# Optimization experiments

Hardware: AMD Instinct MI355X
Metric: run time of the kernel (lower is better)

The kernel has to match this reference:

```python
import jax, jax.numpy as jnp
import numpy as np


def _sliding_window_attention(q, k, v, window_size, padding_mask):
    # q,k,v: [B,H,S,D]; faithful to the torch code incl. clamped scatter_add
    # duplicates at boundaries and the (score==0 -> -inf) quirk.
    B, H, S, D = q.shape
    hw = window_size // 2
    kp = jnp.pad(k, ((0, 0), (0, 0), (hw, hw), (0, 0)))  # zero-pad seq dim
    # window gather positions into padded keys: [S, W+1]
    pos = jnp.arange(S)[:, None] + jnp.arange(window_size + 1)[None, :]
    kw = kp[:, :, pos, :]  # [B,H,S,W+1,D]
    scores = jnp.einsum('bhsd,bhswd->bhsw', q, kw) / jnp.sqrt(jnp.asarray(D, q.dtype))
    # scatter-add into full [B,H,S,S] with clamped column indices (duplicates sum)
    idx = jnp.clip(jnp.arange(S)[:, None] + jnp.arange(-hw, hw + 1)[None, :], 0, S - 1)  # [S,W+1]
    rows = jnp.arange(S)[:, None]
    full = jnp.zeros((B, H, S, S), q.dtype).at[:, :, rows, idx].add(scores)
    neg_inf = jnp.asarray(-jnp.inf, full.dtype)
    full = jnp.where(full == 0.0, neg_inf, full)
    if padding_mask is not None:
        pm = padding_mask[:, None, None, :]  # [B,1,1,S]
        full = jnp.where(pm == 0, neg_inf, full)
        full = jnp.where(jnp.swapaxes(pm, -1, -2) == 0, neg_inf, full)
    att = jax.nn.softmax(full, axis=-1)
    att = jnp.where(jnp.isnan(att), jnp.asarray(0.0, att.dtype), att)
    values = jnp.einsum('bhst,bhtd->bhsd', att, v)
    return values, att


def setup_inputs() -> dict:
    key = jax.random.key(0)
    ks = jax.random.split(key, 5)
    B, S, IN_DIM, E = 2, 2048, 512, 512
    x = jax.random.normal(ks[0], (B, S, IN_DIM), dtype=jnp.float32)
    padding_mask = jnp.ones((B, S), dtype=jnp.int32)
    qkv_w = jax.random.normal(ks[1], (3 * E, IN_DIM), dtype=jnp.float32) * 0.02
    qkv_b = jnp.zeros((3 * E,), dtype=jnp.float32)
    o_w = jax.random.normal(ks[2], (E, E), dtype=jnp.float32) * 0.02
    o_b = jnp.zeros((E,), dtype=jnp.float32)
    return {'x': x, 'padding_mask': padding_mask, 'qkv_w': qkv_w, 'qkv_b': qkv_b,
            'o_w': o_w, 'o_b': o_b, 'window_size': 256, 'num_heads': 8}


def reference(x, padding_mask, qkv_w, qkv_b, o_w, o_b, window_size, num_heads):
    B, S, _ = x.shape
    E3 = qkv_w.shape[0]
    E = E3 // 3
    head_dim = E // num_heads
    qkv = x @ qkv_w.T + qkv_b                         # [B,S,3E]
    qkv = qkv.reshape(B, S, num_heads, 3 * head_dim)
    qkv = jnp.transpose(qkv, (0, 2, 1, 3))            # [B,H,S,3*hd]
    q, k, v = jnp.split(qkv, 3, axis=-1)
    values, _ = _sliding_window_attention(q, k, v, window_size, padding_mask)
    values = jnp.transpose(values, (0, 2, 1, 3)).reshape(B, S, E)
    o = values @ o_w.T + o_b
    return o
```

## Files before the change

### kernel.cpp

```cpp
#include <hip/hip_runtime.h>
#include <hip/hip_bf16.h>
#include <math.h>


typedef __bf16 bf16x8 __attribute__((ext_vector_type(8)));
typedef float f32x4 __attribute__((ext_vector_type(4)));

__device__ __forceinline__ unsigned short f2bf(float f) {
  unsigned u = __float_as_uint(f);
  unsigned r = u + 0x7FFFu + ((u >> 16) & 1u);
  return (unsigned short)(r >> 16);
}

__device__ __forceinline__ void ldsdma16(void* lds, const void* g) {
  __builtin_amdgcn_global_load_lds(
      (const __attribute__((address_space(1))) unsigned int*)g,
      (__attribute__((address_space(3))) unsigned int*)lds, 16, 0, 0);
}

__global__ __launch_bounds__(256) void cvt3_kernel(
    const float* __restrict__ s0, unsigned short* __restrict__ d0, int n0,
    const float* __restrict__ s1, unsigned short* __restrict__ d1, int n1,
    const float* __restrict__ s2, unsigned short* __restrict__ d2, int n2) {
  int i4 = blockIdx.x * 256 + threadIdx.x;
  const int c0 = n0 >> 2, c1 = (n0 + n1) >> 2, c2 = (n0 + n1 + n2) >> 2;
  const float* s; unsigned short* d; int base4;
  if (i4 < c0)      { s = s0; d = d0; base4 = i4; }
  else if (i4 < c1) { s = s1; d = d1; base4 = i4 - c0; }
  else if (i4 < c2) { s = s2; d = d2; base4 = i4 - c1; }
  else return;
  float4 v = ((const float4*)s)[base4];
  ushort4 o;
  o.x = f2bf(v.x); o.y = f2bf(v.y); o.z = f2bf(v.z); o.w = f2bf(v.w);
  ((ushort4*)d)[base4] = o;
}

__global__ __launch_bounds__(256) void gemm_qkv(
    const __hip_bfloat16* __restrict__ A, const __hip_bfloat16* __restrict__ Bw,
    const float* __restrict__ bias,
    __hip_bfloat16* __restrict__ qp, __hip_bfloat16* __restrict__ kpb,
    unsigned short* __restrict__ vtb) {
  __shared__ __hip_bfloat16 As[128 * 32];
  __shared__ __hip_bfloat16 Bs[128 * 32];

  const int tid = threadIdx.x, wave = tid >> 6, lane = tid & 63;
  const int m0 = blockIdx.x * 128, n0 = blockIdx.y * 128;
  const int wm = (wave >> 1) * 64, wn = (wave & 1) * 64;
  const int cl = lane & 15, ko = (lane >> 4) * 8;
  const int srow = wave * 16 + (lane >> 2);
  const int scol = (lane & 3) * 8;

  f32x4 acc[4][4] = {};

  for (int k0 = 0; k0 < 512; k0 += 32) {
    __syncthreads();
    ldsdma16(&As[wave * 512],        A  + (size_t)(m0 + srow) * 512 + k0 + scol);
    ldsdma16(&As[2048 + wave * 512], A  + (size_t)(m0 + 64 + srow) * 512 + k0 + scol);
    ldsdma16(&Bs[wave * 512],        Bw + (size_t)(n0 + srow) * 512 + k0 + scol);
    ldsdma16(&Bs[2048 + wave * 512], Bw + (size_t)(n0 + 64 + srow) * 512 + k0 + scol);
    __syncthreads();

    bf16x8 af[4], bf[4];
#pragma unroll
    for (int i = 0; i < 4; i++)
      af[i] = *(const bf16x8*)(&As[(wm + cl + i * 16) * 32 + ko]);
#pragma unroll
    for (int i = 0; i < 4; i++)
      bf[i] = *(const bf16x8*)(&Bs[(wn + cl + i * 16) * 32 + ko]);
#pragma unroll
    for (int mi = 0; mi < 4; mi++)
#pragma unroll
      for (int ni = 0; ni < 4; ni++)
        acc[mi][ni] = __builtin_amdgcn_mfma_f32_16x16x32_bf16(
            af[mi], bf[ni], acc[mi][ni], 0, 0, 0);
  }

  const int crow = (lane >> 4) * 4;
#pragma unroll
  for (int mi = 0; mi < 4; mi++) {
    const int mb = m0 + wm + mi * 16 + crow;
    const int bq = mb >> 11, sl = mb & 2047;
#pragma unroll
    for (int ni = 0; ni < 4; ni++) {
      const int n = n0 + wn + ni * 16 + cl;
      const int h = n / 192;
      const int rem = n - h * 192;
      const int cat = rem >> 6;
      const int d = rem & 63;
      const float bv = bias[n];
      const size_t bh = (size_t)bq * 8 + h;
      if (cat == 2) {
        ushort4 o;
        o.x = f2bf(acc[mi][ni][0] + bv);
        o.y = f2bf(acc[mi][ni][1] + bv);
        o.z = f2bf(acc[mi][ni][2] + bv);
        o.w = f2bf(acc[mi][ni][3] + bv);
        *(ushort4*)(vtb + bh * 131072 + (sl >> 3) * 512 + d * 8 + (sl & 7)) = o;
      } else {
        __hip_bfloat16* dst = (cat == 0) ? qp : kpb;
        const float sc = (cat == 0) ? 0.18033688011112042f : 1.0f;
#pragma unroll
        for (int r = 0; r < 4; r++)
          dst[(bh * 2048 + sl + r) * 64 + d] =
              __float2bfloat16((acc[mi][ni][r] + bv) * sc);
      }
    }
  }
}

__global__ __launch_bounds__(256) void attn_mfma(
    const __hip_bfloat16* __restrict__ qp, const __hip_bfloat16* __restrict__ kp,
    const __hip_bfloat16* __restrict__ vt, const int* __restrict__ pm,
    __hip_bfloat16* __restrict__ vals) {
  __shared__ __hip_bfloat16 sKP[320 * 72];
  __shared__ float sCM[320];

  const int tid = threadIdx.x, wave = tid >> 6, lane = tid & 63;
  const int bid = blockIdx.x;
  const int s0 = (bid & 31) * 64;
  const int bh = bid >> 5;
  const int b = bh >> 3, h = bh & 7;
  const int t0 = s0 - 128;
  const int cl = lane & 15;
  const int g4 = (lane >> 4) * 4;
  const int ko = (lane >> 4) * 8;

  {
    const int e = (tid & 7) * 8;
#pragma unroll
    for (int i = 0; i < 10; i++) {
      int row = (tid >> 3) + i * 32;
      int t = t0 + row; t = min(max(t, 0), 2047);
      *(uint4*)(&sKP[row * 72 + e]) =
          *(const uint4*)(kp + ((size_t)bh * 2048 + t) * 64 + e);
    }
  }
  for (int c = tid; c < 320; c += 256) {
    int t = t0 + c;
    bool ok = (t >= 0 && t < 2048) && (pm[b * 2048 + t] != 0);
    sCM[c] = ok ? 0.0f : -3.0e38f;
  }
  __syncthreads();

  const __hip_bfloat16* qrow =
      qp + ((size_t)bh * 2048 + s0 + wave * 16 + cl) * 64 + ko;
  bf16x8 aq0 = *(const bf16x8*)(qrow);
  bf16x8 aq1 = *(const bf16x8*)(qrow + 32);

  f32x4 acc[17];
#pragma unroll
  for (int i = 0; i < 17; i++) {
    const int krow = (wave + i) * 16 + cl;
    bf16x8 b0 = *(const bf16x8*)(&sKP[krow * 72 + ko]);
    bf16x8 b1 = *(const bf16x8*)(&sKP[krow * 72 + ko + 32]);
    f32x4 z = {};
    z = __builtin_amdgcn_mfma_f32_16x16x32_bf16(aq0, b0, z, 0, 0, 0);
    acc[i] = __builtin_amdgcn_mfma_f32_16x16x32_bf16(aq1, b1, z, 0, 0, 0);
  }

  float mrow[4] = {-3.0e38f, -3.0e38f, -3.0e38f, -3.0e38f};
#pragma unroll
  for (int i = 0; i < 17; i++) {
    const float ca = sCM[(wave + i) * 16 + cl];
#pragma unroll
    for (int r = 0; r < 4; r++) {
      float sv = acc[i][r] + ca;
      if (i == 0) {
        if (cl < g4 + r) sv = -3.0e38f;
      } else if (i == 16) {
        if (cl > g4 + r) sv = -3.0e38f;
      }
      acc[i][r] = sv;
      mrow[r] = fmaxf(mrow[r], sv);
    }
  }
#pragma unroll
  for (int r = 0; r < 4; r++)
#pragma unroll
    for (int off = 1; off < 16; off <<= 1)
      mrow[r] = fmaxf(mrow[r], __shfl_xor(mrow[r], off));

  float lsum[4] = {0.f, 0.f, 0.f, 0.f};
#pragma unroll
  for (int i = 0; i < 17; i++)
#pragma unroll
    for (int r = 0; r < 4; r++) {
      float p = exp2f(acc[i][r] - mrow[r]);
      acc[i][r] = p;
      lsum[r] += p;
    }
#pragma unroll
  for (int r = 0; r < 4; r++)
#pragma unroll
    for (int off = 1; off < 16; off <<= 1)
      lsum[r] += __shfl_xor(lsum[r], off);

  __syncthreads();

  __hip_bfloat16* sp = sKP + wave * (16 * 296);
  const int roff = (wave & 1) << 4;
#pragma unroll
  for (int i = 0; i < 17; i++) {
    const int rel = i * 16 + cl + roff;
#pragma unroll
    for (int r = 0; r < 4; r++)
      sp[(g4 + r) * 296 + rel] = __float2bfloat16(acc[i][r]);
  }
  {
    const int zc = (wave & 1) ? cl : (272 + cl);
#pragma unroll
    for (int r = 0; r < 4; r++)
      sp[(g4 + r) * 296 + zc] = __float2bfloat16(0.f);
  }

  f32x4 oacc[4] = {};
  const int kb0 = (wave >> 1) * 32;
  const __hip_bfloat16* vbase = vt + (size_t)bh * 131072;
#pragma unroll
  for (int ks = 0; ks < 9; ks++) {
    const int rel = ks * 32 + ko;
    bf16x8 pa = *(const bf16x8*)(&sp[cl * 296 + rel]);
    int tv = t0 + kb0 + rel; tv = min(max(tv, 0), 2040);
    const __hip_bfloat16* vrow = vbase + (tv >> 3) * 512;
#pragma unroll
    for (int ni = 0; ni < 4; ni++) {
      const int d = ni * 16 + cl;
      bf16x8 vb = *(const bf16x8*)(vrow + d * 8);
      oacc[ni] = __builtin_amdgcn_mfma_f32_16x16x32_bf16(pa, vb, oacc[ni], 0, 0, 0);
    }
  }

#pragma unroll
  for (int r = 0; r < 4; r++) {
    float linv = 1.0f / fmaxf(lsum[r], 1e-20f);
    const int qr = wave * 16 + g4 + r;
    if (sCM[qr + 128] != 0.0f) linv = 0.0f;
    const size_t obase = ((size_t)(b * 2048 + s0 + qr)) * 512 + h * 64 + cl;
#pragma unroll
    for (int ni = 0; ni < 4; ni++)
      vals[obase + ni * 16] = __float2bfloat16(oacc[ni][r] * linv);
  }
}

__global__ __launch_bounds__(256) void gemm_out(
    const __hip_bfloat16* __restrict__ A, const __hip_bfloat16* __restrict__ Bw,
    const float* __restrict__ bias, float* __restrict__ C) {
  __shared__ __hip_bfloat16 As[64 * 32];
  __shared__ __hip_bfloat16 Bs[128 * 32];

  const int tid = threadIdx.x, wave = tid >> 6, lane = tid & 63;
  const int m0 = blockIdx.x * 64, n0 = blockIdx.y * 128;
  const int wm = (wave >> 1) * 32, wn = (wave & 1) * 64;
  const int cl = lane & 15, ko = (lane >> 4) * 8;
  const int srow = wave * 16 + (lane >> 2);
  const int scol = (lane & 3) * 8;

  f32x4 acc[2][4] = {};

  for (int k0 = 0; k0 < 512; k0 += 32) {
    __syncthreads();
    ldsdma16(&As[wave * 512],        A  + (size_t)(m0 + srow) * 512 + k0 + scol);
    ldsdma16(&Bs[wave * 512],        Bw + (size_t)(n0 + srow) * 512 + k0 + scol);
    ldsdma16(&Bs[2048 + wave * 512], Bw + (size_t)(n0 + 64 + srow) * 512 + k0 + scol);
    __syncthreads();

    bf16x8 af[2], bf[4];
#pragma unroll
    for (int i = 0; i < 2; i++)
      af[i] = *(const bf16x8*)(&As[(wm + cl + i * 16) * 32 + ko]);
#pragma unroll
    for (int i = 0; i < 4; i++)
      bf[i] = *(const bf16x8*)(&Bs[(wn + cl + i * 16) * 32 + ko]);
#pragma unroll
    for (int mi = 0; mi < 2; mi++)
#pragma unroll
      for (int ni = 0; ni < 4; ni++)
        acc[mi][ni] = __builtin_amdgcn_mfma_f32_16x16x32_bf16(
            af[mi], bf[ni], acc[mi][ni], 0, 0, 0);
  }

  const int crow = (lane >> 4) * 4;
#pragma unroll
  for (int mi = 0; mi < 2; mi++) {
#pragma unroll
    for (int ni = 0; ni < 4; ni++) {
      const int n = n0 + wn + ni * 16 + cl;
      const float bv = bias[n];
      const int mb = m0 + wm + mi * 16 + crow;
#pragma unroll
      for (int r = 0; r < 4; r++)
        C[(size_t)(mb + r) * 512 + n] = acc[mi][ni][r] + bv;
    }
  }
}

extern "C" void kernel_launch(void* const* d_in, const int* in_sizes, int n_in,
                              void* d_out, int out_size, void* d_ws, size_t ws_size,
                              hipStream_t stream) {
  const float* x     = (const float*)d_in[0];
  const int*   pm    = (const int*)d_in[1];
  const float* qkv_w = (const float*)d_in[2];
  const float* qkv_b = (const float*)d_in[3];
  const float* o_w   = (const float*)d_in[4];
  const float* o_b   = (const float*)d_in[5];
  float* out = (float*)d_out;

  __hip_bfloat16* wsb   = (__hip_bfloat16*)d_ws;
  __hip_bfloat16* xb    = wsb;
  __hip_bfloat16* wqkvb = wsb + 2097152;
  __hip_bfloat16* wob   = wsb + 2883584;
  __hip_bfloat16* qp    = wsb + 3145728;
  __hip_bfloat16* kp    = wsb + 5242880;
  __hip_bfloat16* vt    = wsb + 7340032;
  __hip_bfloat16* vals  = wsb + 9437184;

  dim3 blk(256);
  cvt3_kernel<<<dim3(3072), blk, 0, stream>>>(
      x, (unsigned short*)xb, 2097152,
      qkv_w, (unsigned short*)wqkvb, 786432,
      o_w, (unsigned short*)wob, 262144);
  gemm_qkv<<<dim3(32, 12), blk, 0, stream>>>(
      xb, wqkvb, qkv_b, qp, kp, (unsigned short*)vt);
  attn_mfma<<<dim3(512), blk, 0, stream>>>(qp, kp, vt, pm, vals);
  gemm_out<<<dim3(64, 4), blk, 0, stream>>>(vals, wob, o_b, out);
}
```

Baseline: 122.0 us.

## Fuse fp32-to-bf16 conversion into GEMM tile loads, drop separate convert kernel

```diff
diff --git a/kernel.cpp b/kernel.cpp
--- a/kernel.cpp
+++ b/kernel.cpp
@@ -12,61 +12,60 @@
   return (unsigned short)(r >> 16);
 }
 
+__device__ __forceinline__ uint2 pack4(float4 v) {
+  float2 lo2 = {v.x, v.y}, hi2 = {v.z, v.w};
+  __hip_bfloat162 lo = __float22bfloat162_rn(lo2);
+  __hip_bfloat162 hi = __float22bfloat162_rn(hi2);
+  uint2 r;
+  r.x = *(unsigned*)&lo;
+  r.y = *(unsigned*)&hi;
+  return r;
+}
+
 __device__ __forceinline__ void ldsdma16(void* lds, const void* g) {
   __builtin_amdgcn_global_load_lds(
       (const __attribute__((address_space(1))) unsigned int*)g,
       (__attribute__((address_space(3))) unsigned int*)lds, 16, 0, 0);
 }
 
-__global__ __launch_bounds__(256) void cvt3_kernel(
-    const float* __restrict__ s0, unsigned short* __restrict__ d0, int n0,
-    const float* __restrict__ s1, unsigned short* __restrict__ d1, int n1,
-    const float* __restrict__ s2, unsigned short* __restrict__ d2, int n2) {
-  int i4 = blockIdx.x * 256 + threadIdx.x;
-  const int c0 = n0 >> 2, c1 = (n0 + n1) >> 2, c2 = (n0 + n1 + n2) >> 2;
-  const float* s; unsigned short* d; int base4;
-  if (i4 < c0)      { s = s0; d = d0; base4 = i4; }
-  else if (i4 < c1) { s = s1; d = d1; base4 = i4 - c0; }
-  else if (i4 < c2) { s = s2; d = d2; base4 = i4 - c1; }
-  else return;
-  float4 v = ((const float4*)s)[base4];
-  ushort4 o;
-  o.x = f2bf(v.x); o.y = f2bf(v.y); o.z = f2bf(v.z); o.w = f2bf(v.w);
-  ((ushort4*)d)[base4] = o;
-}
-
 __global__ __launch_bounds__(256) void gemm_qkv(
-    const __hip_bfloat16* __restrict__ A, const __hip_bfloat16* __restrict__ Bw,
+    const float* __restrict__ A, const float* __restrict__ Bw,
     const float* __restrict__ bias,
     __hip_bfloat16* __restrict__ qp, __hip_bfloat16* __restrict__ kpb,
     unsigned short* __restrict__ vtb) {
-  __shared__ __hip_bfloat16 As[128 * 32];
-  __shared__ __hip_bfloat16 Bs[128 * 32];
+  __shared__ __hip_bfloat16 As[128 * 40];
+  __shared__ __hip_bfloat16 Bs[128 * 40];
 
   const int tid = threadIdx.x, wave = tid >> 6, lane = tid & 63;
   const int m0 = blockIdx.x * 128, n0 = blockIdx.y * 128;
   const int wm = (wave >> 1) * 64, wn = (wave & 1) * 64;
   const int cl = lane & 15, ko = (lane >> 4) * 8;
-  const int srow = wave * 16 + (lane >> 2);
-  const int scol = (lane & 3) * 8;
+  const int row = tid >> 1;
+  const int half = (tid & 1) * 16;
 
   f32x4 acc[4][4] = {};
 
   for (int k0 = 0; k0 < 512; k0 += 32) {
+    const float* ap = A + (size_t)(m0 + row) * 512 + k0 + half;
+    const float* bp = Bw + (size_t)(n0 + row) * 512 + k0 + half;
+    float4 a0 = ((const float4*)ap)[0], a1 = ((const float4*)ap)[1];
+    float4 a2 = ((const float4*)ap)[2], a3 = ((const float4*)ap)[3];
+    float4 b0 = ((const float4*)bp)[0], b1 = ((const float4*)bp)[1];
+    float4 b2 = ((const float4*)bp)[2], b3 = ((const float4*)bp)[3];
     __syncthreads();
-    ldsdma16(&As[wave * 512],        A  + (size_t)(m0 + srow) * 512 + k0 + scol);
-    ldsdma16(&As[2048 + wave * 512], A  + (size_t)(m0 + 64 + srow) * 512 + k0 + scol);
-    ldsdma16(&Bs[wave * 512],        Bw + (size_t)(n0 + srow) * 512 + k0 + scol);
-    ldsdma16(&Bs[2048 + wave * 512], Bw + (size_t)(n0 + 64 + srow) * 512 + k0 + scol);
+    *(uint4*)(&As[row * 40 + half])     = uint4{pack4(a0).x, pack4(a0).y, pack4(a1).x, pack4(a1).y};
+    *(uint4*)(&As[row * 40 + half + 8]) = uint4{pack4(a2).x, pack4(a2).y, pack4(a3).x, pack4(a3).y};
+    *(uint4*)(&Bs[row * 40 + half])     = uint4{pack4(b0).x, pack4(b0).y, pack4(b1).x, pack4(b1).y};
+    *(uint4*)(&Bs[row * 40 + half + 8]) = uint4{pack4(b2).x, pack4(b2).y, pack4(b3).x, pack4(b3).y};
     __syncthreads();
 
     bf16x8 af[4], bf[4];
 #pragma unroll
     for (int i = 0; i < 4; i++)
-      af[i] = *(const bf16x8*)(&As[(wm + cl + i * 16) * 32 + ko]);
+      af[i] = *(const bf16x8*)(&As[(wm + cl + i * 16) * 40 + ko]);
 #pragma unroll
     for (int i = 0; i < 4; i++)
-      bf[i] = *(const bf16x8*)(&Bs[(wn + cl + i * 16) * 32 + ko]);
+      bf[i] = *(const bf16x8*)(&Bs[(wn + cl + i * 16) * 40 + ko]);
 #pragma unroll
     for (int mi = 0; mi < 4; mi++)
 #pragma unroll
@@ -243,10 +242,10 @@
 }
 
 __global__ __launch_bounds__(256) void gemm_out(
-    const __hip_bfloat16* __restrict__ A, const __hip_bfloat16* __restrict__ Bw,
+    const __hip_bfloat16* __restrict__ A, const float* __restrict__ Bw,
     const float* __restrict__ bias, float* __restrict__ C) {
   __shared__ __hip_bfloat16 As[64 * 32];
-  __shared__ __hip_bfloat16 Bs[128 * 32];
+  __shared__ __hip_bfloat16 Bs[128 * 40];
 
   const int tid = threadIdx.x, wave = tid >> 6, lane = tid & 63;
   const int m0 = blockIdx.x * 64, n0 = blockIdx.y * 128;
@@ -254,14 +253,19 @@
   const int cl = lane & 15, ko = (lane >> 4) * 8;
   const int srow = wave * 16 + (lane >> 2);
   const int scol = (lane & 3) * 8;
+  const int row = tid >> 1;
+  const int half = (tid & 1) * 16;
 
   f32x4 acc[2][4] = {};
 
   for (int k0 = 0; k0 < 512; k0 += 32) {
+    const float* bp = Bw + (size_t)(n0 + row) * 512 + k0 + half;
+    float4 b0 = ((const float4*)bp)[0], b1 = ((const float4*)bp)[1];
+    float4 b2 = ((const float4*)bp)[2], b3 = ((const float4*)bp)[3];
     __syncthreads();
-    ldsdma16(&As[wave * 512],        A  + (size_t)(m0 + srow) * 512 + k0 + scol);
-    ldsdma16(&Bs[wave * 512],        Bw + (size_t)(n0 + srow) * 512 + k0 + scol);
-    ldsdma16(&Bs[2048 + wave * 512], Bw + (size_t)(n0 + 64 + srow) * 512 + k0 + scol);
+    ldsdma16(&As[wave * 512], A + (size_t)(m0 + srow) * 512 + k0 + scol);
+    *(uint4*)(&Bs[row * 40 + half])     = uint4{pack4(b0).x, pack4(b0).y, pack4(b1).x, pack4(b1).y};
+    *(uint4*)(&Bs[row * 40 + half + 8]) = uint4{pack4(b2).x, pack4(b2).y, pack4(b3).x, pack4(b3).y};
     __syncthreads();
 
     bf16x8 af[2], bf[4];
@@ -270,7 +274,7 @@
       af[i] = *(const bf16x8*)(&As[(wm + cl + i * 16) * 32 + ko]);
 #pragma unroll
     for (int i = 0; i < 4; i++)
-      bf[i] = *(const bf16x8*)(&Bs[(wn + cl + i * 16) * 32 + ko]);
+      bf[i] = *(const bf16x8*)(&Bs[(wn + cl + i * 16) * 40 + ko]);
 #pragma unroll
     for (int mi = 0; mi < 2; mi++)
 #pragma unroll
@@ -305,22 +309,15 @@
   const float* o_b   = (const float*)d_in[5];
   float* out = (float*)d_out;
 
-  __hip_bfloat16* wsb   = (__hip_bfloat16*)d_ws;
-  __hip_bfloat16* xb    = wsb;
-  __hip_bfloat16* wqkvb = wsb + 2097152;
-  __hip_bfloat16* wob   = wsb + 2883584;
-  __hip_bfloat16* qp    = wsb + 3145728;
-  __hip_bfloat16* kp    = wsb + 5242880;
-  __hip_bfloat16* vt    = wsb + 7340032;
-  __hip_bfloat16* vals  = wsb + 9437184;
+  __hip_bfloat16* wsb  = (__hip_bfloat16*)d_ws;
+  __hip_bfloat16* qp   = wsb;
+  __hip_bfloat16* kp   = wsb + 2097152;
+  __hip_bfloat16* vt   = wsb + 4194304;
+  __hip_bfloat16* vals = wsb + 6291456;
 
   dim3 blk(256);
-  cvt3_kernel<<<dim3(3072), blk, 0, stream>>>(
-      x, (unsigned short*)xb, 2097152,
-      qkv_w, (unsigned short*)wqkvb, 786432,
-      o_w, (unsigned short*)wob, 262144);
   gemm_qkv<<<dim3(32, 12), blk, 0, stream>>>(
-      xb, wqkvb, qkv_b, qp, kp, (unsigned short*)vt);
+      x, qkv_w, qkv_b, qp, kp, (unsigned short*)vt);
   attn_mfma<<<dim3(512), blk, 0, stream>>>(qp, kp, vt, pm, vals);
-  gemm_out<<<dim3(64, 4), blk, 0, stream>>>(vals, wob, o_b, out);
-}
+  gemm_out<<<dim3(64, 4), blk, 0, stream>>>(vals, o_w, o_b, out);
+}
```

Measured after the change: 136.0 us. +11.5%, slower.
